# Optimization experiments

Hardware: AMD Instinct MI355X
Metric: run time of the kernel (lower is better)

## Reference

```python
import jax, jax.numpy as jnp
import numpy as np


def setup_inputs() -> dict:
    key = jax.random.key(0)
    ks = jax.random.split(key, 8)
    B, C, T, F = 2, 2, 500, 129
    H, D = 16, 100  # hidden_channels, delay
    return {
        "x_mic": jax.random.normal(ks[0], (B, C, T, F), jnp.float32),
        "x_ref": jax.random.normal(ks[1], (B, C, T, F), jnp.float32),
        "w_mic": jax.random.normal(ks[2], (H, C), jnp.float32) * 0.5,
        "b_mic": jax.random.normal(ks[3], (H,), jnp.float32) * 0.1,
        "w_ref": jax.random.normal(ks[4], (H, C), jnp.float32) * 0.5,
        "b_ref": jax.random.normal(ks[5], (H,), jnp.float32) * 0.1,
        "w_conv": jax.random.normal(ks[6], (1, H, 5, 3), jnp.float32) * 0.05,
        "b_conv": jax.random.normal(ks[7], (1,), jnp.float32) * 0.1,
        "delay": D,
    }


def reference(x_mic, x_ref, w_mic, b_mic, w_ref, b_ref, w_conv, b_conv, delay):
    # x_mic, x_ref: (B, C, T, F)
    B, C, T, F = x_mic.shape
    # 1x1 convs == per-(t,f) channel mixing
    Q = jnp.einsum('bctf,hc->bhtf', x_mic, w_mic) + b_mic[None, :, None, None]
    K = jnp.einsum('bctf,hc->bhtf', x_ref, w_ref) + b_ref[None, :, None, None]

    # unfold: zero-pad (delay-1) frames at the start of T, take sliding windows
    # window index d at output frame t maps to K[t - (delay-1) + d]
    idx = jnp.arange(T)[:, None] + jnp.arange(delay)[None, :]  # (T, delay) indices into padded T
    Kp = jnp.pad(K, ((0, 0), (0, 0), (delay - 1, 0), (0, 0)))
    Ku = Kp[:, :, idx, :]  # (B, H, T, delay, F)

    # windowed cross-correlation over frequency
    V = jnp.einsum('bhtf,bhtdf->bhtd', Q, Ku)  # (B, H, T, delay)

    # (5,3) conv, causal pad 4 along T (height), symmetric pad 1 along delay (width)
    V = jax.lax.conv_general_dilated(
        V, w_conv, window_strides=(1, 1), padding=[(4, 0), (1, 1)],
        dimension_numbers=('NCHW', 'OIHW', 'NCHW'))
    V = V + b_conv[None, :, None, None]  # (B, 1, T, delay)

    A = jax.nn.softmax(V[:, 0], axis=-1)  # (B, T, delay) attention over delays

    # unfold raw x_ref the same way and take delay-weighted sum
    Rp = jnp.pad(x_ref, ((0, 0), (0, 0), (delay - 1, 0), (0, 0)))
    Ru = Rp[:, :, idx, :]  # (B, C, T, delay, F)
    y = jnp.einsum('bctdf,btd->bctf', Ru, A)  # (B, C, T, F)
    return y
```

## Files before the change

### kernel.cpp

```cpp
#include <hip/hip_runtime.h>
#include <math.h>

constexpr int NB = 2;
constexpr int NC = 2;
constexpr int NT = 500;
constexpr int NF = 129;
constexpr int NH = 16;
constexpr int ND = 100;

constexpr int VTS = NT + 4;
constexpr int VDS = ND + 2;
constexpr size_t VELEMS = (size_t)NB * NH * VTS * VDS;

typedef _Float16 f16;
typedef _Float16 f16x4 __attribute__((ext_vector_type(4)));
typedef float    f32x4 __attribute__((ext_vector_type(4)));

constexpr int TT   = 16;
constexpr int NTT  = (NT + TT - 1) / TT;
constexpr int LROWS = 144;
constexpr int LSTR  = 148;

__global__ __launch_bounds__(256) void v_kernel(
    const float* __restrict__ x_mic, const float* __restrict__ x_ref,
    const float* __restrict__ w_mic, const float* __restrict__ b_mic,
    const float* __restrict__ w_ref, const float* __restrict__ b_ref,
    float* __restrict__ Vp)
{
    __shared__ f16 Lds[LROWS * LSTR];

    const int tid = threadIdx.x;
    const int tt  = blockIdx.x & 31;
    const int bh  = blockIdx.x >> 5;
    const int h = bh & 15, b = bh >> 4;
    const int ts = tt * TT;
    const int US = ts - (ND - 1);

    const float wm0 = w_mic[h*NC+0], wm1 = w_mic[h*NC+1], bm = b_mic[h];
    const float wr0 = w_ref[h*NC+0], wr1 = w_ref[h*NC+1], br = b_ref[h];

    const float* xm0 = x_mic + ((size_t)b*NC + 0) * NT * NF;
    const float* xm1 = x_mic + ((size_t)b*NC + 1) * NT * NF;
    const float* xr0 = x_ref + ((size_t)b*NC + 0) * NT * NF;
    const float* xr1 = x_ref + ((size_t)b*NC + 1) * NT * NF;

    const int w = tid >> 6;
    const int l = tid & 63;

    for (int rr = 0; rr < 36; ++rr) {
        const int r = w + 4 * rr;
        const bool isK = (r < 128);
        const int row = isK ? (US + r) : (ts + r - 128);
        const bool valid = (row >= 0) && (row < NT);
        const float* p0 = isK ? xr0 : xm0;
        const float* p1 = isK ? xr1 : xm1;
        const float w0 = isK ? wr0 : wm0;
        const float w1 = isK ? wr1 : wm1;
        const float bb = isK ? br  : bm;
        const size_t base = (size_t)row * NF;
        f16* ldsrow = Lds + r * LSTR;

        float v0 = 0.f, v1 = 0.f;
        if (valid) {
            v0 = w0 * p0[base + l]      + w1 * p1[base + l]      + bb;
            v1 = w0 * p0[base + l + 64] + w1 * p1[base + l + 64] + bb;
        }
        ldsrow[l]      = (f16)v0;
        ldsrow[l + 64] = (f16)v1;
        if (l < LSTR - 128) {
            const int c = 128 + l;
            float v2 = (valid && c < NF) ? (w0 * p0[base + c] + w1 * p1[base + c] + bb) : 0.f;
            ldsrow[c] = (f16)v2;
        }
    }
    __syncthreads();

    const int lr = l & 15;
    const int lk = l >> 4;
    f32x4 acc0 = {0.f, 0.f, 0.f, 0.f};
    f32x4 acc1 = {0.f, 0.f, 0.f, 0.f};

    #pragma unroll
    for (int kk = 0; kk < 9; ++kk) {
        const int fo = 16 * kk + 4 * lk;
        f16x4 a  = *(const f16x4*)&Lds[(128 + lr) * LSTR + fo];
        f16x4 b0 = *(const f16x4*)&Lds[(32*w      + lr) * LSTR + fo];
        f16x4 b1 = *(const f16x4*)&Lds[(32*w + 16 + lr) * LSTR + fo];
        acc0 = __builtin_amdgcn_mfma_f32_16x16x16f16(a, b0, acc0, 0, 0, 0);
        acc1 = __builtin_amdgcn_mfma_f32_16x16x16f16(a, b1, acc1, 0, 0, 0);
    }

    float* Vb = Vp + (size_t)bh * VTS * VDS;
    #pragma unroll
    for (int j = 0; j < 4; ++j) {
        const int t_loc = 4 * lk + j;
        const int t_g = ts + t_loc;
        if (t_g < NT) {
            const int u0 = 32*w + lr;
            const int d0 = u0 - t_loc;
            if (d0 >= 0 && d0 < ND) Vb[(size_t)(t_g + 4) * VDS + d0 + 1] = acc0[j];
            const int u1 = u0 + 16;
            const int d1 = u1 - t_loc;
            if (d1 >= 0 && d1 < ND) Vb[(size_t)(t_g + 4) * VDS + d1 + 1] = acc1[j];
        }
    }
}

__global__ __launch_bounds__(128) void cs_kernel(
    const float* __restrict__ Vp, const float* __restrict__ w_conv,
    const float* __restrict__ b_conv, float* __restrict__ A)
{
    const int t = blockIdx.x % NT;
    const int b = blockIdx.x / NT;
    const int tid = threadIdx.x;
    const int d = tid;

    float s = 0.f;
    if (d < ND) {
        #pragma unroll 4
        for (int h = 0; h < NH; ++h) {
            const float* Vb = Vp + ((size_t)(b*NH + h) * VTS + t) * VDS + d;
            const float* wh = w_conv + h * 15;
            #pragma unroll
            for (int kt = 0; kt < 5; ++kt)
                #pragma unroll
                for (int kd = 0; kd < 3; ++kd)
                    s += wh[kt*3 + kd] * Vb[kt*VDS + kd];
        }
        s += b_conv[0];
    }

    __shared__ float red[4];
    float m = (d < ND) ? s : -3.4e38f;
    #pragma unroll
    for (int o = 32; o > 0; o >>= 1) m = fmaxf(m, __shfl_down(m, o, 64));
    if ((tid & 63) == 0) red[tid >> 6] = m;
    __syncthreads();
    m = fmaxf(red[0], red[1]);
    float e = (d < ND) ? __expf(s - m) : 0.f;
    float sm = e;
    #pragma unroll
    for (int o = 32; o > 0; o >>= 1) sm += __shfl_down(sm, o, 64);
    if ((tid & 63) == 0) red[2 + (tid >> 6)] = sm;
    __syncthreads();
    const float inv = 1.f / (red[2] + red[3]);
    if (d < ND) A[((size_t)b*NT + t) * ND + d] = e * inv;
}

__global__ __launch_bounds__(256) void y_kernel(
    const float* __restrict__ x_ref, const float* __restrict__ A,
    float* __restrict__ y)
{
    const int idx = blockIdx.x * 256 + threadIdx.x;
    if (idx >= NB * NC * NT * NF) return;
    const int f  = idx % NF;
    const int r  = idx / NF;
    const int t  = r % NT;
    const int bc = r / NT;
    const int b  = bc >> 1;

    const float* At = A + ((size_t)b * NT + t) * ND;
    const float* X  = x_ref + (size_t)bc * NT * NF + f;
    const int d0 = (t >= ND - 1) ? 0 : (ND - 1 - t);

    const float* Xp = X + (size_t)(t + d0 - (ND - 1)) * NF;
    float acc = 0.f;
    #pragma unroll 4
    for (int d = d0; d < ND; ++d) {
        acc += At[d] * Xp[0];
        Xp += NF;
    }
    y[idx] = acc;
}

extern "C" void kernel_launch(void* const* d_in, const int* in_sizes, int n_in,
                              void* d_out, int out_size, void* d_ws, size_t ws_size,
                              hipStream_t stream)
{
    const float* x_mic  = (const float*)d_in[0];
    const float* x_ref  = (const float*)d_in[1];
    const float* w_mic  = (const float*)d_in[2];
    const float* b_mic  = (const float*)d_in[3];
    const float* w_ref  = (const float*)d_in[4];
    const float* b_ref  = (const float*)d_in[5];
    const float* w_conv = (const float*)d_in[6];
    const float* b_conv = (const float*)d_in[7];
    float* y = (float*)d_out;

    float* Vp = (float*)d_ws;
    float* A  = Vp + VELEMS;

    hipMemsetAsync(Vp, 0, VELEMS * sizeof(float), stream);

    v_kernel<<<dim3(NB * NH * NTT), dim3(256), 0, stream>>>(
        x_mic, x_ref, w_mic, b_mic, w_ref, b_ref, Vp);
    cs_kernel<<<dim3(NB * NT), dim3(128), 0, stream>>>(Vp, w_conv, b_conv, A);
    const int nOut = NB * NC * NT * NF;
    y_kernel<<<dim3((nOut + 255) / 256), dim3(256), 0, stream>>>(x_ref, A, y);
}
```

Baseline: 123.2 us.

## Fuse conv-softmax with weighted sum and drop the workspace memset

```diff
diff --git a/kernel.cpp b/kernel.cpp
--- a/kernel.cpp
+++ b/kernel.cpp
@@ -104,16 +104,30 @@
             if (d1 >= 0 && d1 < ND) Vb[(size_t)(t_g + 4) * VDS + d1 + 1] = acc1[j];
         }
     }
+
+    if (tid < 32) {
+        const int rr = tid >> 1, side = tid & 1;
+        const int t_g = ts + rr;
+        if (t_g < NT)
+            Vb[(size_t)(t_g + 4) * VDS + (side ? (VDS - 1) : 0)] = 0.f;
+    }
+    if (tt == 0) {
+        for (int q = tid; q < 4 * VDS; q += 256) Vb[q] = 0.f;
+    }
 }
 
-__global__ __launch_bounds__(128) void cs_kernel(
+__global__ __launch_bounds__(256) void csy_kernel(
     const float* __restrict__ Vp, const float* __restrict__ w_conv,
-    const float* __restrict__ b_conv, float* __restrict__ A)
+    const float* __restrict__ b_conv, const float* __restrict__ x_ref,
+    float* __restrict__ y)
 {
     const int t = blockIdx.x % NT;
     const int b = blockIdx.x / NT;
     const int tid = threadIdx.x;
     const int d = tid;
+
+    __shared__ float Alds[ND];
+    __shared__ float red[4];
 
     float s = 0.f;
     if (d < ND) {
@@ -130,47 +144,38 @@
         s += b_conv[0];
     }
 
-    __shared__ float red[4];
-    float m = (d < ND) ? s : -3.4e38f;
-    #pragma unroll
-    for (int o = 32; o > 0; o >>= 1) m = fmaxf(m, __shfl_down(m, o, 64));
-    if ((tid & 63) == 0) red[tid >> 6] = m;
-    __syncthreads();
-    m = fmaxf(red[0], red[1]);
-    float e = (d < ND) ? __expf(s - m) : 0.f;
-    float sm = e;
-    #pragma unroll
-    for (int o = 32; o > 0; o >>= 1) sm += __shfl_down(sm, o, 64);
-    if ((tid & 63) == 0) red[2 + (tid >> 6)] = sm;
+    if (tid < 128) {
+        float m = (d < ND) ? s : -3.4e38f;
+        #pragma unroll
+        for (int o = 32; o > 0; o >>= 1) m = fmaxf(m, __shfl_down(m, o, 64));
+        if ((tid & 63) == 0) red[tid >> 6] = m;
+    }
+    __syncthreads();
+    const float m = fmaxf(red[0], red[1]);
+    const float e = (d < ND) ? __expf(s - m) : 0.f;
+    if (tid < 128) {
+        float sm = e;
+        #pragma unroll
+        for (int o = 32; o > 0; o >>= 1) sm += __shfl_down(sm, o, 64);
+        if ((tid & 63) == 0) red[2 + (tid >> 6)] = sm;
+    }
     __syncthreads();
     const float inv = 1.f / (red[2] + red[3]);
-    if (d < ND) A[((size_t)b*NT + t) * ND + d] = e * inv;
-}
-
-__global__ __launch_bounds__(256) void y_kernel(
-    const float* __restrict__ x_ref, const float* __restrict__ A,
-    float* __restrict__ y)
-{
-    const int idx = blockIdx.x * 256 + threadIdx.x;
-    if (idx >= NB * NC * NT * NF) return;
-    const int f  = idx % NF;
-    const int r  = idx / NF;
-    const int t  = r % NT;
-    const int bc = r / NT;
-    const int b  = bc >> 1;
-
-    const float* At = A + ((size_t)b * NT + t) * ND;
-    const float* X  = x_ref + (size_t)bc * NT * NF + f;
+    if (d < ND) Alds[d] = e * inv;
+    __syncthreads();
+
     const int d0 = (t >= ND - 1) ? 0 : (ND - 1 - t);
-
-    const float* Xp = X + (size_t)(t + d0 - (ND - 1)) * NF;
-    float acc = 0.f;
-    #pragma unroll 4
-    for (int d = d0; d < ND; ++d) {
-        acc += At[d] * Xp[0];
-        Xp += NF;
-    }
-    y[idx] = acc;
+    for (int o = tid; o < NC * NF; o += 256) {
+        const int c = o / NF, f = o - c * NF;
+        const float* X = x_ref + ((size_t)(b*NC + c) * NT + (t + d0 - (ND - 1))) * NF + f;
+        float acc = 0.f;
+        #pragma unroll 4
+        for (int dd = d0; dd < ND; ++dd) {
+            acc += Alds[dd] * X[0];
+            X += NF;
+        }
+        y[((size_t)(b*NC + c) * NT + t) * NF + f] = acc;
+    }
 }
 
 extern "C" void kernel_launch(void* const* d_in, const int* in_sizes, int n_in,
@@ -188,13 +193,9 @@
     float* y = (float*)d_out;
 
     float* Vp = (float*)d_ws;
-    float* A  = Vp + VELEMS;
-
-    hipMemsetAsync(Vp, 0, VELEMS * sizeof(float), stream);
 
     v_kernel<<<dim3(NB * NH * NTT), dim3(256), 0, stream>>>(
         x_mic, x_ref, w_mic, b_mic, w_ref, b_ref, Vp);
-    cs_kernel<<<dim3(NB * NT), dim3(128), 0, stream>>>(Vp, w_conv, b_conv, A);
-    const int nOut = NB * NC * NT * NF;
-    y_kernel<<<dim3((nOut + 255) / 256), dim3(256), 0, stream>>>(x_ref, A, y);
+    csy_kernel<<<dim3(NB * NT), dim3(256), 0, stream>>>(
+        Vp, w_conv, b_conv, x_ref, y);
 }
```

New measurement: 121.0 us. No clear change (-1.7%).
